# Optimization experiments

Hardware: AMD Instinct MI355X
Metric: run time of the kernel (lower is better)

Reference implementation:

```python
import jax, jax.numpy as jnp
import numpy as np

EPS = 1e-12  # torch F.normalize eps


def unfold(x, ksize, pad):
    # torch F.unfold equivalent: [B,C,H,W] -> [B, C*k*k, L], channel-major ordering
    patches = jax.lax.conv_general_dilated_patches(
        x, (ksize, ksize), (1, 1), [(pad, pad), (pad, pad)],
        dimension_numbers=('NCHW', 'OIHW', 'NCHW'))
    B, CKK, Hp, Wp = patches.shape
    return patches.reshape(B, CKK, Hp * Wp)


def fold(patches, C, ksize, H, W, pad):
    # torch F.fold equivalent (stride 1): overlap-add of [B, C*k*k, H*W] -> [B,C,H,W]
    B = patches.shape[0]
    p = patches.reshape(B, C, ksize, ksize, H, W)
    out = jnp.zeros((B, C, H + 2 * pad, W + 2 * pad), patches.dtype)
    for di in range(ksize):
        for dj in range(ksize):
            out = out.at[:, :, di:di + H, dj:dj + W].add(p[:, :, di, dj])
    return out[:, :, pad:pad + H, pad:pad + W]


def setup_inputs() -> dict:
    key = jax.random.key(0)
    ks = jax.random.split(key, 4)
    B, C, H, W = 2, 512, 64, 64
    D, CIN = 256, 512 * 9  # embed: Linear(tdim*8*3*3 -> tdim*4), tdim=64
    return {
        'query': jax.random.normal(ks[0], (B, C, H, W), dtype=jnp.float32),
        'key': jax.random.normal(ks[1], (B, C, H, W), dtype=jnp.float32),
        'value': jax.random.normal(ks[2], (B, C, H, W), dtype=jnp.float32),
        'W_embed': jax.random.normal(ks[3], (D, CIN), dtype=jnp.float32) * 0.02,
        'k': 3,
    }


def reference(query, key, value, W_embed, k):
    B, Cv, H, W = value.shape
    # patch embed: unfold -> linear (no bias)
    q_unf = unfold(query, k, k // 2)                       # [B, C*k*k, L]
    k_unf = unfold(key, k, k // 2)                         # [B, C*k*k, L]
    k_emb = jnp.einsum('bcl,dc->bld', k_unf, W_embed)      # [B, L, D]
    q_emb = jnp.einsum('bcl,dc->bdl', q_unf, W_embed)      # [B, D, L]
    # cosine correlation
    k_n = k_emb / jnp.maximum(jnp.linalg.norm(k_emb, axis=2, keepdims=True), EPS)
    q_n = q_emb / jnp.maximum(jnp.linalg.norm(q_emb, axis=1, keepdims=True), EPS)
    corr = jnp.einsum('bld,bdm->blm', k_n, q_n)            # [B, L_key, L_query]
    corr_value = jnp.max(corr, axis=1)                     # [B, L]
    corr_argmax = jnp.argmax(corr, axis=1)                 # [B, L]
    # swap(V=value, idx=corr_argmax, s=1, k=k)
    s = 1
    temph = s * k + H * s - H - s                          # = k - 1
    tempw = s * k + W * s - W - s
    ph = max(temph // 2 + temph % 2, 1)
    pw = max(tempw // 2 + tempw % 2, 1)
    v_unf = unfold(value, k, ph)                           # [B, Cv*k*k, L] (ph==pw for square)
    t_unf = jnp.take_along_axis(v_unf, corr_argmax[:, None, :], axis=2)
    divisor = fold(jnp.ones_like(t_unf), Cv, k, H, W, ph)
    T = fold(t_unf, Cv, k, H, W, ph) / divisor             # [B, Cv, H, W]
    S = corr_value.reshape(B, 1, H, W)
    return S, T
```

## Files before the change

kernel.cpp:

```cpp
#include <hip/hip_runtime.h>
#include <hip/hip_bf16.h>
#include <stdint.h>
#include <math.h>

#define BB 2
#define CC 512
#define HH 64
#define WW 64
#define LL 4096
#define DD 256
#define CIN 4608
#define NG 144

typedef _Float16 half_t;
typedef __attribute__((ext_vector_type(8))) _Float16 f16x8;
typedef __attribute__((ext_vector_type(4))) _Float16 f16x4;
typedef __attribute__((ext_vector_type(4))) float f32x4;

__global__ __launch_bounds__(256) void presplit(const float* __restrict__ query,
                                                const float* __restrict__ key,
                                                char* __restrict__ img_ts) {
    __shared__ float tile[32][65];
    int img = blockIdx.y;
    int y   = blockIdx.x;
    const float* src = ((img >> 1) ? key : query) + (size_t)(img & 1) * CC * LL + y * WW;
    char* dstbase = img_ts + ((size_t)img * 64 + y) * (16 * 64 * 128);
    int t = threadIdx.x;
    int xl = t & 63, c4 = t >> 6;
    int xw = t >> 2, fsw = t & 3;
    for (int cc = 0; cc < 16; ++cc) {
#pragma unroll
        for (int j = 0; j < 8; ++j) {
            int cl = c4 + j * 4;
            tile[cl][xl] = src[(size_t)(cc * 32 + cl) * LL + xl];
        }
        __syncthreads();
        f16x8 h8, l8;
#pragma unroll
        for (int j = 0; j < 8; ++j) {
            float v = tile[fsw * 8 + j][xw];
            half_t h = (half_t)v;
            h8[j] = h; l8[j] = (half_t)(v - (float)h);
        }
        char* p = dstbase + (size_t)cc * 8192 + xw * 128;
        int swz = (xw & 7) << 4;
        *(f16x8*)(p + ((fsw * 16) ^ swz)) = h8;
        *(f16x8*)(p + ((64 + fsw * 16) ^ swz)) = l8;
        __syncthreads();
    }
}

__global__ __launch_bounds__(256) void splitW2b(const float* __restrict__ W,
                                                char* __restrict__ Wst) {
    int i = blockIdx.x * 256 + threadIdx.x;
    if (i >= NG * DD * 4) return;
    int g  = i >> 10;
    int r  = i & 1023;
    int d  = r >> 2;
    int fs = r & 3;
    int cc = g / 9, o = g - cc * 9;
    const float* src = W + (size_t)d * CIN;
    f16x8 h8, l8;
#pragma unroll
    for (int j = 0; j < 8; j++) {
        float w = src[(cc * 32 + fs * 8 + j) * 9 + o];
        half_t h = (half_t)w;
        h8[j] = h;
        l8[j] = (half_t)(w - (float)h);
    }
    size_t base = (size_t)g * 32768 + d * 128;
    int sw = (d & 7) << 4;
    *(f16x8*)(Wst + base + ((fs * 16) ^ sw)) = h8;
    *(f16x8*)(Wst + base + ((64 + fs * 16) ^ sw)) = l8;
}

#define GATE() do { asm volatile("s_waitcnt vmcnt(0) lgkmcnt(0)" ::: "memory"); \
                    __builtin_amdgcn_s_barrier(); \
                    __builtin_amdgcn_sched_barrier(0); } while (0)

__global__ __launch_bounds__(512) void embed_mfma(const char* __restrict__ img_ts,
                                                  const char* __restrict__ Wst,
                                                  const char* __restrict__ zp,
                                                  char* __restrict__ qemb,
                                                  char* __restrict__ kemb) {
    __shared__ char sW[2][32768];
    __shared__ char sB[2][32768];
    __shared__ float red[4][64];
    __shared__ float invn[64];

    int iid = blockIdx.y;
    int b = iid & 1, type = iid >> 1;
    int y = blockIdx.x;
    int l0 = y * 64;
    int t = threadIdx.x;
    int w = t >> 6, lane = t & 63;
    int wr = w >> 1, wc = w & 1;
    int fr = lane & 15, fs = lane >> 4;

    const char* imgb = img_ts + (size_t)iid * (64 * 16 * 64 * 128);
    const char *ps0, *ps1, *ps2, *ps3;
    int pb0, pb1, pb2, pb3;
#define PREP(c, PS, PB)                                                 \
    {                                                                   \
        int q = (c) * 512 + t;                                          \
        int di = q / 528;                                               \
        int rem = q - di * 528;                                         \
        int xi = rem >> 3, sub = rem & 7;                               \
        int xg = xi - 1, yg = y + di - 1;                               \
        bool ok = (di < 3) && (yg >= 0) && (yg < 64) && (xg >= 0) && (xg < 64); \
        PS = ok ? imgb + (size_t)yg * 131072 + (size_t)xg * 128 + (sub * 16) \
                : zp + ((q & 255) * 16);                                \
        PB = ok ? 8192 : 0;                                             \
    }
    PREP(0, ps0, pb0); PREP(1, ps1, pb1); PREP(2, ps2, pb2); PREP(3, ps3, pb3);

    const char* pW = Wst;

#define DMAW(dst)                                                       \
    do {                                                                \
        _Pragma("unroll")                                               \
        for (int c = 0; c < 4; c++)                                     \
            __builtin_amdgcn_global_load_lds(                           \
                (const __attribute__((address_space(1))) void*)(pW + c * 8192 + t * 16), \
                (__attribute__((address_space(3))) void*)((dst) + c * 8192 + t * 16), 16, 0, 0); \
        pW += 32768;                                                    \
    } while (0)

#define DMAB(dst)                                                       \
    do {                                                                \
        __builtin_amdgcn_global_load_lds((const __attribute__((address_space(1))) void*)ps0, \
            (__attribute__((address_space(3))) void*)((dst) + t * 16), 16, 0, 0); \
        __builtin_amdgcn_global_load_lds((const __attribute__((address_space(1))) void*)ps1, \
            (__attribute__((address_space(3))) void*)((dst) + 8192 + t * 16), 16, 0, 0); \
        __builtin_amdgcn_global_load_lds((const __attribute__((address_space(1))) void*)ps2, \
            (__attribute__((address_space(3))) void*)((dst) + 16384 + t * 16), 16, 0, 0); \
        __builtin_amdgcn_global_load_lds((const __attribute__((address_space(1))) void*)ps3, \
            (__attribute__((address_space(3))) void*)((dst) + 24576 + t * 16), 16, 0, 0); \
        ps0 += pb0; ps1 += pb1; ps2 += pb2; ps3 += pb3;                 \
    } while (0)

#define READA(AH, AL, wbuf)                                             \
    do {                                                                \
        _Pragma("unroll")                                               \
        for (int rg = 0; rg < 4; rg++) {                                \
            int dl = wr * 64 + rg * 16 + fr;                            \
            int sw_ = (dl & 7) << 4;                                    \
            const char* rowp = (const char*)(wbuf) + dl * 128;          \
            AH[rg] = *(const f16x8*)(rowp + ((fs * 16) ^ sw_));         \
            AL[rg] = *(const f16x8*)(rowp + ((64 + fs * 16) ^ sw_));    \
        }                                                               \
    } while (0)

#define READB(BH, BL, bbuf, di_, dj_)                                   \
    do {                                                                \
        _Pragma("unroll")                                               \
        for (int cg = 0; cg < 2; cg++) {                                \
            int xi = wc * 32 + cg * 16 + fr + (dj_);                    \
            int sw_ = ((xi - 1) & 7) << 4;                              \
            const char* rowp = (const char*)(bbuf) + (di_) * 8448 + xi * 128; \
            BH[cg] = *(const f16x8*)(rowp + ((fs * 16) ^ sw_));         \
            BL[cg] = *(const f16x8*)(rowp + ((64 + fs * 16) ^ sw_));    \
        }                                                               \
    } while (0)

#define DOMFMA(AH, AL, BH, BL)                                          \
    do {                                                                \
        _Pragma("unroll")                                               \
        for (int rg = 0; rg < 4; rg++)                                  \
            _Pragma("unroll")                                           \
            for (int cg = 0; cg < 2; cg++)                              \
                acc[rg][cg] = __builtin_amdgcn_mfma_f32_16x16x32_f16(AH[rg], BH[cg], acc[rg][cg], 0, 0, 0); \
        _Pragma("unroll")                                               \
        for (int rg = 0; rg < 4; rg++)                                  \
            _Pragma("unroll")                                           \
            for (int cg = 0; cg < 2; cg++) {                            \
                acc[rg][cg] = __builtin_amdgcn_mfma_f32_16x16x32_f16(AH[rg], BL[cg], acc[rg][cg], 0, 0, 0); \
                acc[rg][cg] = __builtin_amdgcn_mfma_f32_16x16x32_f16(AL[rg], BH[cg], acc[rg][cg], 0, 0, 0); \
            }                                                           \
    } while (0)

    f32x4 acc[4][2];
#pragma unroll
    for (int rg = 0; rg < 4; rg++)
#pragma unroll
        for (int cg = 0; cg < 2; cg++) acc[rg][cg] = (f32x4){0.f, 0.f, 0.f, 0.f};

    f16x8 ah0[4], al0[4], bh0[2], bl0[2];
    f16x8 ah1[4], al1[4], bh1[2], bl1[2];

    char* wb0 = &sW[0][0]; char* wb1 = &sW[1][0];
    char* b0 = &sB[0][0];  char* b1 = &sB[1][0];

    DMAB(b0);
    DMAW(wb0);
    GATE();
    READA(ah0, al0, wb0);
    READB(bh0, bl0, b0, 0, 0);
    DMAW(wb1);
    DMAB(b1);
    __builtin_amdgcn_sched_barrier(0);

    int o = 1, issued = 2;
    char* bcur = b0;
    char* bnext = b0;

#define HALF(AHr, ALr, BHr, BLr, WRD, WWR, AHm, ALm, BHm, BLm)          \
    GATE();                                                             \
    READA(AHr, ALr, WRD);                                               \
    {                                                                   \
        int di_ = (o >= 6) ? 2 : (o >= 3) ? 1 : 0;                      \
        int dj_ = o - di_ * 3;                                          \
        READB(BHr, BLr, bcur, di_, dj_);                                \
    }                                                                   \
    DMAW(WWR);                                                          \
    if (o == 0 && issued < 16) {                                        \
        DMAB(bnext);                                                    \
        bnext = (bnext == b0) ? b1 : b0;                                \
        issued++;                                                       \
    }                                                                   \
    o++; if (o == 9) { o = 0; bcur = (bcur == b0) ? b1 : b0; }          \
    __builtin_amdgcn_sched_barrier(0);                                  \
    DOMFMA(AHm, ALm, BHm, BLm);

#pragma unroll 1
    for (int i = 0; i < 71; ++i) {
        HALF(ah1, al1, bh1, bl1, wb1, wb0, ah0, al0, bh0, bl0)
        HALF(ah0, al0, bh0, bl0, wb0, wb1, ah1, al1, bh1, bl1)
    }
    GATE();
    READA(ah1, al1, wb1);
    READB(bh1, bl1, bcur, 2, 2);
    __builtin_amdgcn_sched_barrier(0);
    DOMFMA(ah0, al0, bh0, bl0);
    DOMFMA(ah1, al1, bh1, bl1);
#undef HALF

    float ss[2] = {0.f, 0.f};
#pragma unroll
    for (int rg = 0; rg < 4; rg++)
#pragma unroll
        for (int cg = 0; cg < 2; cg++)
#pragma unroll
            for (int r = 0; r < 4; r++) ss[cg] += acc[rg][cg][r] * acc[rg][cg][r];
#pragma unroll
    for (int cg = 0; cg < 2; cg++) {
        ss[cg] += __shfl_xor(ss[cg], 16);
        ss[cg] += __shfl_xor(ss[cg], 32);
    }
    if (lane < 16) {
        red[wr][wc * 32 + lane] = ss[0];
        red[wr][wc * 32 + 16 + lane] = ss[1];
    }
    __syncthreads();
    if (t < 64) {
        float s = red[0][t] + red[1][t] + red[2][t] + red[3][t];
        invn[t] = 1.0f / fmaxf(sqrtf(s), 1e-12f);
    }
    __syncthreads();

    char* e = (type == 0) ? qemb : kemb;
#pragma unroll
    for (int cg = 0; cg < 2; cg++) {
        int lloc = wc * 32 + cg * 16 + fr;
        float sc = invn[lloc];
        int l = l0 + lloc;
        char* rowp = e + ((size_t)b * LL + l) * 1024;
        int swb = (l & 7) << 4;
#pragma unroll
        for (int rg = 0; rg < 4; rg++) {
            int d0 = wr * 64 + rg * 16 + fs * 4;
            f16x4 h4, l4;
#pragma unroll
            for (int r = 0; r < 4; r++) {
                float v = acc[rg][cg][r] * sc;
                half_t h = (half_t)v;
                h4[r] = h;
                l4[r] = (half_t)(v - (float)h);
            }
            int itb = d0 >> 5;
            int fsc = (d0 >> 3) & 3;
            int sub = (d0 & 7) * 2;
            *(f16x4*)(rowp + itb * 128 + ((fsc * 16) ^ swb) + sub) = h4;
            *(f16x4*)(rowp + itb * 128 + ((64 + fsc * 16) ^ swb) + sub) = l4;
        }
    }
#undef PREP
#undef DMAW
#undef DMAB
#undef READA
#undef READB
#undef DOMFMA
}

__global__ void init_packed(unsigned long long* p, int n) {
    int i = blockIdx.x * 256 + threadIdx.x;
    if (i < n) p[i] = 0ull;
}

__global__ __launch_bounds__(256, 2) void corr_max_mfma(const char* __restrict__ kemb,
                                                        const char* __restrict__ qemb,
                                                        unsigned long long* __restrict__ packed) {
    __shared__ char sA[2][16384];
    __shared__ char sBq[2][16384];

    int b  = blockIdx.z;
    int l0 = blockIdx.y * 128;
    int m0 = blockIdx.x * 128;
    int t  = threadIdx.x;
    int w = t >> 6, lane = t & 63;
    int wr = w >> 1, wc = w & 1;
    int fr = lane & 15, fs = lane >> 4;

    const char* Abase = kemb + ((size_t)b * LL + l0) * 1024;
    const char* Bbase = qemb + ((size_t)b * LL + m0) * 1024;

    f32x4 acc[4][4];
#pragma unroll
    for (int i = 0; i < 4; i++)
#pragma unroll
        for (int j = 0; j < 4; j++) acc[i][j] = (f32x4){0.f, 0.f, 0.f, 0.f};

#define DMA2(bufi, itv)                                                   \
    do {                                                                  \
        _Pragma("unroll")                                                 \
        for (int c = 0; c < 4; c++) {                                     \
            int idx = c * 4096 + t * 16;                                  \
            int row = idx >> 7, offb = idx & 127;                         \
            __builtin_amdgcn_global_load_lds(                             \
                (const __attribute__((address_space(1))) void*)(Abase + (size_t)row * 1024 + (itv) * 128 + offb), \
                (__attribute__((address_space(3))) void*)(&sA[bufi][idx]), 16, 0, 0); \
        }                                                                 \
        _Pragma("unroll")                                                 \
        for (int c = 0; c < 4; c++) {                                     \
            int idx = c * 4096 + t * 16;                                  \
            int row = idx >> 7, offb = idx & 127;                         \
            __builtin_amdgcn_global_load_lds(                             \
                (const __attribute__((address_space(1))) void*)(Bbase + (size_t)row * 1024 + (itv) * 128 + offb), \
                (__attribute__((address_space(3))) void*)(&sBq[bufi][idx]), 16, 0, 0); \
        }                                                                 \
    } while (0)

    DMA2(0, 0);

    f16x8 ah[4], al[4], bh[4], bl[4];
    for (int it = 0; it < 8; ++it) {
        asm volatile("s_waitcnt vmcnt(0) lgkmcnt(0)" ::: "memory");
        __builtin_amdgcn_s_barrier();
        __builtin_amdgcn_sched_barrier(0);
        if (it < 7) DMA2((it + 1) & 1, it + 1);
        __builtin_amdgcn_sched_barrier(0);
        const char* sa = sA[it & 1];
        const char* sb = sBq[it & 1];
#pragma unroll
        for (int rg = 0; rg < 4; rg++) {
            int r = wr * 64 + rg * 16 + fr;
            const char* rp = sa + r * 128;
            int sw_ = (r & 7) << 4;
            ah[rg] = *(const f16x8*)(rp + ((fs * 16) ^ sw_));
            al[rg] = *(const f16x8*)(rp + ((64 + fs * 16) ^ sw_));
        }
#pragma unroll
        for (int cg = 0; cg < 4; cg++) {
            int r = wc * 64 + cg * 16 + fr;
            const char* rp = sb + r * 128;
            int sw_ = (r & 7) << 4;
            bh[cg] = *(const f16x8*)(rp + ((fs * 16) ^ sw_));
            bl[cg] = *(const f16x8*)(rp + ((64 + fs * 16) ^ sw_));
        }
#pragma unroll
        for (int rg = 0; rg < 4; rg++)
#pragma unroll
            for (int cg = 0; cg < 4; cg++)
                acc[rg][cg] = __builtin_amdgcn_mfma_f32_16x16x32_f16(ah[rg], bh[cg], acc[rg][cg], 0, 0, 0);
#pragma unroll
        for (int rg = 0; rg < 4; rg++)
#pragma unroll
            for (int cg = 0; cg < 4; cg++) {
                acc[rg][cg] = __builtin_amdgcn_mfma_f32_16x16x32_f16(ah[rg], bl[cg], acc[rg][cg], 0, 0, 0);
                acc[rg][cg] = __builtin_amdgcn_mfma_f32_16x16x32_f16(al[rg], bh[cg], acc[rg][cg], 0, 0, 0);
            }
    }
#undef DMA2

#pragma unroll
    for (int cg = 0; cg < 4; cg++) {
        unsigned long long best = 0ull;
#pragma unroll
        for (int rg = 0; rg < 4; rg++) {
#pragma unroll
            for (int r = 0; r < 4; r++) {
                unsigned u = __float_as_uint(acc[rg][cg][r]);
                u = (u & 0x80000000u) ? ~u : (u | 0x80000000u);
                int l = l0 + wr * 64 + rg * 16 + fs * 4 + r;
                unsigned long long p = ((unsigned long long)u << 32) | (unsigned)(4095 - l);
                best = (p > best) ? p : best;
            }
        }
        unsigned long long oo;
        oo = __shfl_xor(best, 16); best = (oo > best) ? oo : best;
        oo = __shfl_xor(best, 32); best = (oo > best) ? oo : best;
        if (lane < 16)
            atomicMax(&packed[(size_t)b * LL + m0 + wc * 64 + cg * 16 + lane], best);
    }
}

__global__ void decode_packed(const unsigned long long* __restrict__ packed,
                              float* __restrict__ S_out, int* __restrict__ arg) {
    int i = blockIdx.x * 256 + threadIdx.x;
    if (i < BB * LL) {
        unsigned long long p = packed[i];
        unsigned u = (unsigned)(p >> 32);
        unsigned bits = (u & 0x80000000u) ? (u & 0x7FFFFFFFu) : ~u;
        S_out[i] = __uint_as_float(bits);
        arg[i] = 4095 - (int)(unsigned)(p & 0xFFFFFFFFull);
    }
}

__global__ __launch_bounds__(256) void transpose_mat(const float* __restrict__ src,
                                                     float* __restrict__ dst,
                                                     int R, int Cc) {
    __shared__ float tile[32][33];
    size_t boff = (size_t)blockIdx.z * R * Cc;
    int bx = blockIdx.x;
    int by = blockIdx.y;
    int tx = threadIdx.x & 31;
    int ty = threadIdx.x >> 5;
    const float* s = src + boff;
    float* d = dst + boff;
#pragma unroll
    for (int i = 0; i < 4; i++) {
        int r = by * 32 + ty + i * 8;
        int c = bx * 32 + tx;
        tile[ty + i * 8][tx] = s[(size_t)r * Cc + c];
    }
    __syncthreads();
#pragma unroll
    for (int i = 0; i < 4; i++) {
        int c = bx * 32 + ty + i * 8;
        int r = by * 32 + tx;
        d[(size_t)c * R + r] = tile[tx][ty + i * 8];
    }
}

__global__ __launch_bounds__(256) void gather_fold(const float* __restrict__ value_t,
                                                   const int* __restrict__ arg,
                                                   float* __restrict__ T_t) {
    int b = blockIdx.y;
    int pix = blockIdx.x;
    int y = pix >> 6, x = pix & 63;
    int t = threadIdx.x;
    float2 acc = make_float2(0.f, 0.f);
    int cnty = (y == 0 || y == HH - 1) ? 2 : 3;
    int cntx = (x == 0 || x == WW - 1) ? 2 : 3;
    const int* ab = arg + b * LL;
    const float* vb = value_t + (size_t)b * LL * CC;
#pragma unroll
    for (int di = 0; di < 3; di++) {
        int my = y + 1 - di;
        if (my < 0 || my >= HH) continue;
#pragma unroll
        for (int dj = 0; dj < 3; dj++) {
            int mx = x + 1 - dj;
            if (mx < 0 || mx >= WW) continue;
            int a = ab[my * WW + mx];
            int ay = a >> 6, ax = a & 63;
            int vy = ay + di - 1, vx = ax + dj - 1;
            if (vy < 0 || vy >= HH || vx < 0 || vx >= WW) continue;
            float2 v = *(const float2*)&vb[((size_t)(vy * WW + vx)) * CC + t * 2];
            acc.x += v.x; acc.y += v.y;
        }
    }
    float inv = 1.0f / (float)(cnty * cntx);
    acc.x *= inv; acc.y *= inv;
    *(float2*)&T_t[((size_t)b * LL + pix) * CC + t * 2] = acc;
}

extern "C" void kernel_launch(void* const* d_in, const int* in_sizes, int n_in,
                              void* d_out, int out_size, void* d_ws, size_t ws_size,
                              hipStream_t stream) {
    const float* query = (const float*)d_in[0];
    const float* key   = (const float*)d_in[1];
    const float* value = (const float*)d_in[2];
    const float* Wemb  = (const float*)d_in[3];

    float* out   = (float*)d_out;
    float* S_out = out;
    float* T_out = out + BB * LL;

    char* ws = (char*)d_ws;
    char* img_ts = ws;
    char* Wst    = ws + 33554432;
    char* qemb   = ws + 38273024;
    char* kemb   = ws + 46661632;
    unsigned long long* packed = (unsigned long long*)(ws + 55050240);
    char* zp     = ws + 55115776;
    int*  arg    = (int*)(ws + 55119872);
    float* val_t = (float*)ws;
    float* T_t   = (float*)(ws + 16777216);

    init_packed   <<<dim3(34), 256, 0, stream>>>(packed, 8704);
    presplit      <<<dim3(64, 4), 256, 0, stream>>>(query, key, img_ts);
    splitW2b      <<<dim3(576), 256, 0, stream>>>(Wemb, Wst);
    embed_mfma    <<<dim3(64, 4), 512, 0, stream>>>(img_ts, Wst, zp, qemb, kemb);
    corr_max_mfma <<<dim3(32, 32, 2), 256, 0, stream>>>(kemb, qemb, packed);
    decode_packed <<<dim3(32), 256, 0, stream>>>(packed, S_out, arg);
    transpose_mat <<<dim3(128, 16, 2), 256, 0, stream>>>(value, val_t, CC, LL);
    gather_fold   <<<dim3(4096, 2), 256, 0, stream>>>(val_t, arg, T_t);
    transpose_mat <<<dim3(16, 128, 2), 256, 0, stream>>>(T_t, T_out, LL, CC);
}
```

Baseline: 229.3 us.

## Split embed GEMM over K with two-row tiles and separate normalize kernel

The embed GEMM now gives each block two image rows (128 positions) and half of the channel range (split-K over blockIdx.z). Each block writes fp32 partial sums to a workspace buffer, and a new norm_split kernel adds the two halves, L2-normalizes and writes the hi/lo fp16 split layout. The main loop also drops the double-buffered register ping-pong for a simpler single-stage loop with a barrier after each step. The aim is more B-tile reuse per W load and the same block count with a larger per-block tile. The cost is an extra kernel launch, a round trip of the fp32 partials through memory, and less overlap between LDS reads and MFMA.

```diff
diff --git a/kernel.cpp b/kernel.cpp
--- a/kernel.cpp
+++ b/kernel.cpp
@@ -78,115 +78,113 @@
                     __builtin_amdgcn_s_barrier(); \
                     __builtin_amdgcn_sched_barrier(0); } while (0)
 
-__global__ __launch_bounds__(512) void embed_mfma(const char* __restrict__ img_ts,
-                                                  const char* __restrict__ Wst,
-                                                  const char* __restrict__ zp,
-                                                  char* __restrict__ qemb,
-                                                  char* __restrict__ kemb) {
+__global__ __launch_bounds__(512, 1) void embed_mfma(const char* __restrict__ img_ts,
+                                                     const char* __restrict__ Wst,
+                                                     const char* __restrict__ zp,
+                                                     float* __restrict__ part) {
     __shared__ char sW[2][32768];
-    __shared__ char sB[2][32768];
-    __shared__ float red[4][64];
-    __shared__ float invn[64];
+    __shared__ char sB[2][33792];
 
     int iid = blockIdx.y;
-    int b = iid & 1, type = iid >> 1;
-    int y = blockIdx.x;
-    int l0 = y * 64;
+    int ks  = blockIdx.z;
+    int lt  = blockIdx.x;
+    int y0  = lt * 2;
     int t = threadIdx.x;
     int w = t >> 6, lane = t & 63;
     int wr = w >> 1, wc = w & 1;
     int fr = lane & 15, fs = lane >> 4;
 
-    const char* imgb = img_ts + (size_t)iid * (64 * 16 * 64 * 128);
-    const char *ps0, *ps1, *ps2, *ps3;
-    int pb0, pb1, pb2, pb3;
-#define PREP(c, PS, PB)                                                 \
+    const char* imgb = img_ts + (size_t)iid * (64 * 16 * 64 * 128) + (size_t)ks * 65536;
+    const char *ps0, *ps1, *ps2, *ps3, *ps4;
+    int pb0, pb1, pb2, pb3, pb4;
+#define PREP(qv, PS, PB)                                                \
     {                                                                   \
-        int q = (c) * 512 + t;                                          \
-        int di = q / 528;                                               \
-        int rem = q - di * 528;                                         \
+        int q = (qv);                                                   \
+        int ri = q / 528;                                               \
+        int rem = q - ri * 528;                                         \
         int xi = rem >> 3, sub = rem & 7;                               \
-        int xg = xi - 1, yg = y + di - 1;                               \
-        bool ok = (di < 3) && (yg >= 0) && (yg < 64) && (xg >= 0) && (xg < 64); \
-        PS = ok ? imgb + (size_t)yg * 131072 + (size_t)xg * 128 + (sub * 16) \
+        int xg = xi - 1, yg = y0 - 1 + ri;                              \
+        bool ok = (yg >= 0) && (yg < 64) && (xg >= 0) && (xg < 64);     \
+        PS = ok ? imgb + (size_t)yg * 131072 + (size_t)xg * 128 + sub * 16 \
                 : zp + ((q & 255) * 16);                                \
         PB = ok ? 8192 : 0;                                             \
     }
-    PREP(0, ps0, pb0); PREP(1, ps1, pb1); PREP(2, ps2, pb2); PREP(3, ps3, pb3);
-
-    const char* pW = Wst;
+    PREP(t, ps0, pb0); PREP(512 + t, ps1, pb1); PREP(1024 + t, ps2, pb2);
+    PREP(1536 + t, ps3, pb3); PREP(2048 + t, ps4, pb4);
+
+    const char* pW = Wst + (size_t)ks * 72 * 32768;
+
+#define GLL(src, dst)                                                   \
+    __builtin_amdgcn_global_load_lds(                                   \
+        (const __attribute__((address_space(1))) void*)(src),           \
+        (__attribute__((address_space(3))) void*)(dst), 16, 0, 0)
 
 #define DMAW(dst)                                                       \
     do {                                                                \
         _Pragma("unroll")                                               \
         for (int c = 0; c < 4; c++)                                     \
-            __builtin_amdgcn_global_load_lds(                           \
-                (const __attribute__((address_space(1))) void*)(pW + c * 8192 + t * 16), \
-                (__attribute__((address_space(3))) void*)((dst) + c * 8192 + t * 16), 16, 0, 0); \
+            GLL(pW + c * 8192 + t * 16, (dst) + c * 8192 + t * 16);     \
         pW += 32768;                                                    \
     } while (0)
 
 #define DMAB(dst)                                                       \
     do {                                                                \
-        __builtin_amdgcn_global_load_lds((const __attribute__((address_space(1))) void*)ps0, \
-            (__attribute__((address_space(3))) void*)((dst) + t * 16), 16, 0, 0); \
-        __builtin_amdgcn_global_load_lds((const __attribute__((address_space(1))) void*)ps1, \
-            (__attribute__((address_space(3))) void*)((dst) + 8192 + t * 16), 16, 0, 0); \
-        __builtin_amdgcn_global_load_lds((const __attribute__((address_space(1))) void*)ps2, \
-            (__attribute__((address_space(3))) void*)((dst) + 16384 + t * 16), 16, 0, 0); \
-        __builtin_amdgcn_global_load_lds((const __attribute__((address_space(1))) void*)ps3, \
-            (__attribute__((address_space(3))) void*)((dst) + 24576 + t * 16), 16, 0, 0); \
-        ps0 += pb0; ps1 += pb1; ps2 += pb2; ps3 += pb3;                 \
+        GLL(ps0, (dst) + t * 16);                                       \
+        GLL(ps1, (dst) + 8192 + t * 16);                                \
+        GLL(ps2, (dst) + 16384 + t * 16);                               \
+        GLL(ps3, (dst) + 24576 + t * 16);                               \
+        if (t < 64) GLL(ps4, (dst) + 32768 + t * 16);                   \
+        ps0 += pb0; ps1 += pb1; ps2 += pb2; ps3 += pb3; ps4 += pb4;     \
     } while (0)
 
-#define READA(AH, AL, wbuf)                                             \
+#define READA(wbuf)                                                     \
     do {                                                                \
         _Pragma("unroll")                                               \
         for (int rg = 0; rg < 4; rg++) {                                \
             int dl = wr * 64 + rg * 16 + fr;                            \
             int sw_ = (dl & 7) << 4;                                    \
             const char* rowp = (const char*)(wbuf) + dl * 128;          \
-            AH[rg] = *(const f16x8*)(rowp + ((fs * 16) ^ sw_));         \
-            AL[rg] = *(const f16x8*)(rowp + ((64 + fs * 16) ^ sw_));    \
+            ah[rg] = *(const f16x8*)(rowp + ((fs * 16) ^ sw_));         \
+            al[rg] = *(const f16x8*)(rowp + ((64 + fs * 16) ^ sw_));    \
         }                                                               \
     } while (0)
 
-#define READB(BH, BL, bbuf, di_, dj_)                                   \
+#define READB(bbuf, di_, dj_)                                           \
     do {                                                                \
+        int ri = wc + (di_);                                            \
         _Pragma("unroll")                                               \
-        for (int cg = 0; cg < 2; cg++) {                                \
-            int xi = wc * 32 + cg * 16 + fr + (dj_);                    \
+        for (int cg = 0; cg < 4; cg++) {                                \
+            int xi = cg * 16 + fr + (dj_);                              \
             int sw_ = ((xi - 1) & 7) << 4;                              \
-            const char* rowp = (const char*)(bbuf) + (di_) * 8448 + xi * 128; \
-            BH[cg] = *(const f16x8*)(rowp + ((fs * 16) ^ sw_));         \
-            BL[cg] = *(const f16x8*)(rowp + ((64 + fs * 16) ^ sw_));    \
+            const char* rowp = (const char*)(bbuf) + ri * 8448 + xi * 128; \
+            bh[cg] = *(const f16x8*)(rowp + ((fs * 16) ^ sw_));         \
+            bl[cg] = *(const f16x8*)(rowp + ((64 + fs * 16) ^ sw_));    \
         }                                                               \
     } while (0)
 
-#define DOMFMA(AH, AL, BH, BL)                                          \
+#define DOMFMA()                                                        \
     do {                                                                \
         _Pragma("unroll")                                               \
         for (int rg = 0; rg < 4; rg++)                                  \
             _Pragma("unroll")                                           \
-            for (int cg = 0; cg < 2; cg++)                              \
-                acc[rg][cg] = __builtin_amdgcn_mfma_f32_16x16x32_f16(AH[rg], BH[cg], acc[rg][cg], 0, 0, 0); \
+            for (int cg = 0; cg < 4; cg++)                              \
+                acc[rg][cg] = __builtin_amdgcn_mfma_f32_16x16x32_f16(ah[rg], bh[cg], acc[rg][cg], 0, 0, 0); \
         _Pragma("unroll")                                               \
         for (int rg = 0; rg < 4; rg++)                                  \
             _Pragma("unroll")                                           \
-            for (int cg = 0; cg < 2; cg++) {                            \
-                acc[rg][cg] = __builtin_amdgcn_mfma_f32_16x16x32_f16(AH[rg], BL[cg], acc[rg][cg], 0, 0, 0); \
-                acc[rg][cg] = __builtin_amdgcn_mfma_f32_16x16x32_f16(AL[rg], BH[cg], acc[rg][cg], 0, 0, 0); \
+            for (int cg = 0; cg < 4; cg++) {                            \
+                acc[rg][cg] = __builtin_amdgcn_mfma_f32_16x16x32_f16(ah[rg], bl[cg], acc[rg][cg], 0, 0, 0); \
+                acc[rg][cg] = __builtin_amdgcn_mfma_f32_16x16x32_f16(al[rg], bh[cg], acc[rg][cg], 0, 0, 0); \
             }                                                           \
     } while (0)
 
-    f32x4 acc[4][2];
+    f32x4 acc[4][4];
 #pragma unroll
     for (int rg = 0; rg < 4; rg++)
 #pragma unroll
-        for (int cg = 0; cg < 2; cg++) acc[rg][cg] = (f32x4){0.f, 0.f, 0.f, 0.f};
-
-    f16x8 ah0[4], al0[4], bh0[2], bl0[2];
-    f16x8 ah1[4], al1[4], bh1[2], bl1[2];
+        for (int cg = 0; cg < 4; cg++) acc[rg][cg] = (f32x4){0.f, 0.f, 0.f, 0.f};
+
+    f16x8 ah[4], al[4], bh[4], bl[4];
 
     char* wb0 = &sW[0][0]; char* wb1 = &sW[1][0];
     char* b0 = &sB[0][0];  char* b1 = &sB[1][0];
@@ -194,102 +192,106 @@
     DMAB(b0);
     DMAW(wb0);
     GATE();
-    READA(ah0, al0, wb0);
-    READB(bh0, bl0, b0, 0, 0);
-    DMAW(wb1);
-    DMAB(b1);
-    __builtin_amdgcn_sched_barrier(0);
-
-    int o = 1, issued = 2;
-    char* bcur = b0;
-    char* bnext = b0;
-
-#define HALF(AHr, ALr, BHr, BLr, WRD, WWR, AHm, ALm, BHm, BLm)          \
-    GATE();                                                             \
-    READA(AHr, ALr, WRD);                                               \
-    {                                                                   \
-        int di_ = (o >= 6) ? 2 : (o >= 3) ? 1 : 0;                      \
-        int dj_ = o - di_ * 3;                                          \
-        READB(BHr, BLr, bcur, di_, dj_);                                \
-    }                                                                   \
-    DMAW(WWR);                                                          \
-    if (o == 0 && issued < 16) {                                        \
-        DMAB(bnext);                                                    \
-        bnext = (bnext == b0) ? b1 : b0;                                \
-        issued++;                                                       \
-    }                                                                   \
-    o++; if (o == 9) { o = 0; bcur = (bcur == b0) ? b1 : b0; }          \
-    __builtin_amdgcn_sched_barrier(0);                                  \
-    DOMFMA(AHm, ALm, BHm, BLm);
+
+    char* wcur = wb0; char* wnext = wb1;
+    char* bcur = b0;  char* bnext = b1;
+    int o = 0, ccl = 0;
 
 #pragma unroll 1
-    for (int i = 0; i < 71; ++i) {
-        HALF(ah1, al1, bh1, bl1, wb1, wb0, ah0, al0, bh0, bl0)
-        HALF(ah0, al0, bh0, bl0, wb0, wb1, ah1, al1, bh1, bl1)
-    }
-    GATE();
-    READA(ah1, al1, wb1);
-    READB(bh1, bl1, bcur, 2, 2);
-    __builtin_amdgcn_sched_barrier(0);
-    DOMFMA(ah0, al0, bh0, bl0);
-    DOMFMA(ah1, al1, bh1, bl1);
-#undef HALF
-
-    float ss[2] = {0.f, 0.f};
+    for (int g = 0; g < 72; ++g) {
+        int di_ = (o >= 6) ? 2 : (o >= 3) ? 1 : 0;
+        int dj_ = o - di_ * 3;
+        READA(wcur);
+        READB(bcur, di_, dj_);
+        if (g < 71) DMAW(wnext);
+        if (o == 8 && ccl < 7) DMAB(bnext);
+        __builtin_amdgcn_sched_barrier(0);
+        DOMFMA();
+        GATE();
+        { char* tp = wcur; wcur = wnext; wnext = tp; }
+        if (o == 8) { char* tp = bcur; bcur = bnext; bnext = tp; o = 0; ccl++; }
+        else o++;
+    }
+
+    float* pt = part + (((size_t)iid * 32 + lt) * 2 + ks) * 32768;
 #pragma unroll
     for (int rg = 0; rg < 4; rg++)
 #pragma unroll
-        for (int cg = 0; cg < 2; cg++)
-#pragma unroll
-            for (int r = 0; r < 4; r++) ss[cg] += acc[rg][cg][r] * acc[rg][cg][r];
-#pragma unroll
-    for (int cg = 0; cg < 2; cg++) {
-        ss[cg] += __shfl_xor(ss[cg], 16);
-        ss[cg] += __shfl_xor(ss[cg], 32);
-    }
-    if (lane < 16) {
-        red[wr][wc * 32 + lane] = ss[0];
-        red[wr][wc * 32 + 16 + lane] = ss[1];
-    }
-    __syncthreads();
-    if (t < 64) {
-        float s = red[0][t] + red[1][t] + red[2][t] + red[3][t];
-        invn[t] = 1.0f / fmaxf(sqrtf(s), 1e-12f);
-    }
-    __syncthreads();
-
-    char* e = (type == 0) ? qemb : kemb;
-#pragma unroll
-    for (int cg = 0; cg < 2; cg++) {
-        int lloc = wc * 32 + cg * 16 + fr;
-        float sc = invn[lloc];
-        int l = l0 + lloc;
-        char* rowp = e + ((size_t)b * LL + l) * 1024;
-        int swb = (l & 7) << 4;
-#pragma unroll
-        for (int rg = 0; rg < 4; rg++) {
+        for (int cg = 0; cg < 4; cg++) {
+            int l = wc * 64 + cg * 16 + fr;
             int d0 = wr * 64 + rg * 16 + fs * 4;
-            f16x4 h4, l4;
-#pragma unroll
-            for (int r = 0; r < 4; r++) {
-                float v = acc[rg][cg][r] * sc;
-                half_t h = (half_t)v;
-                h4[r] = h;
-                l4[r] = (half_t)(v - (float)h);
-            }
-            int itb = d0 >> 5;
-            int fsc = (d0 >> 3) & 3;
-            int sub = (d0 & 7) * 2;
-            *(f16x4*)(rowp + itb * 128 + ((fsc * 16) ^ swb) + sub) = h4;
-            *(f16x4*)(rowp + itb * 128 + ((64 + fsc * 16) ^ swb) + sub) = l4;
-        }
-    }
+#pragma unroll
+            for (int r = 0; r < 4; r++)
+                pt[(d0 + r) * 128 + l] = acc[rg][cg][r];
+        }
 #undef PREP
+#undef GLL
 #undef DMAW
 #undef DMAB
 #undef READA
 #undef READB
 #undef DOMFMA
+}
+
+__global__ __launch_bounds__(256) void norm_split(const float* __restrict__ part,
+                                                  char* __restrict__ qemb,
+                                                  char* __restrict__ kemb) {
+    __shared__ float sm[4][64];
+    __shared__ float invn[64];
+    __shared__ char stage[64][1040];
+
+    int iid = blockIdx.y;
+    int bx  = blockIdx.x;
+    int lt  = bx >> 1, lh2 = bx & 1;
+    const float* p0 = part + (((size_t)iid * 32 + lt) * 2 + 0) * 32768 + lh2 * 64;
+    const float* p1 = p0 + 32768;
+    int t = threadIdx.x;
+    int ll = t & 63, dq = t >> 6;
+
+    float sq = 0.f;
+    for (int dd = 0; dd < 64; ++dd) {
+        int d = dq * 64 + dd;
+        float v = p0[d * 128 + ll] + p1[d * 128 + ll];
+        sq += v * v;
+    }
+    sm[dq][ll] = sq;
+    __syncthreads();
+    if (t < 64) {
+        float s = sm[0][t] + sm[1][t] + sm[2][t] + sm[3][t];
+        invn[t] = 1.0f / fmaxf(sqrtf(s), 1e-12f);
+    }
+    __syncthreads();
+
+    float sc = invn[ll];
+    int swb = (ll & 7) << 4;
+    for (int oc = 0; oc < 8; ++oc) {
+        int d0 = dq * 64 + oc * 8;
+        f16x8 h8, l8;
+#pragma unroll
+        for (int j = 0; j < 8; ++j) {
+            int d = d0 + j;
+            float v = (p0[d * 128 + ll] + p1[d * 128 + ll]) * sc;
+            half_t h = (half_t)v;
+            h8[j] = h;
+            l8[j] = (half_t)(v - (float)h);
+        }
+        int itb = d0 >> 5;
+        int fsc = (d0 >> 3) & 3;
+        *(f16x8*)&stage[ll][itb * 128 + ((fsc * 16) ^ swb)] = h8;
+        *(f16x8*)&stage[ll][itb * 128 + ((64 + fsc * 16) ^ swb)] = l8;
+    }
+    __syncthreads();
+
+    int b = iid & 1, type = iid >> 1;
+    char* e = (type ? kemb : qemb);
+    int rr = t >> 2, c0 = t & 3;
+    char* erow = e + ((size_t)b * LL + lt * 128 + lh2 * 64 + rr) * 1024;
+    const char* srow = &stage[rr][0];
+#pragma unroll
+    for (int c = 0; c < 16; ++c) {
+        int cj = c0 + c * 4;
+        *(float4*)(erow + cj * 16) = *(const float4*)(srow + cj * 16);
+    }
 }
 
 __global__ void init_packed(unsigned long long* p, int n) {
@@ -488,20 +490,22 @@
     float* T_out = out + BB * LL;
 
     char* ws = (char*)d_ws;
-    char* img_ts = ws;
-    char* Wst    = ws + 33554432;
-    char* qemb   = ws + 38273024;
-    char* kemb   = ws + 46661632;
-    unsigned long long* packed = (unsigned long long*)(ws + 55050240);
-    char* zp     = ws + 55115776;
-    int*  arg    = (int*)(ws + 55119872);
-    float* val_t = (float*)ws;
-    float* T_t   = (float*)(ws + 16777216);
+    char*  img_ts = ws;
+    char*  Wst    = ws + 33554432;
+    float* part   = (float*)(ws + 38273024);
+    char*  qemb   = ws + 71827456;
+    char*  kemb   = ws + 80216064;
+    unsigned long long* packed = (unsigned long long*)(ws + 88604672);
+    char*  zp     = ws + 88670208;
+    int*   arg    = (int*)(ws + 88674304);
+    float* val_t  = (float*)(ws + 38273024);
+    float* T_t    = (float*)(ws + 38273024 + 16777216);
 
     init_packed   <<<dim3(34), 256, 0, stream>>>(packed, 8704);
     presplit      <<<dim3(64, 4), 256, 0, stream>>>(query, key, img_ts);
     splitW2b      <<<dim3(576), 256, 0, stream>>>(Wemb, Wst);
-    embed_mfma    <<<dim3(64, 4), 512, 0, stream>>>(img_ts, Wst, zp, qemb, kemb);
+    embed_mfma    <<<dim3(32, 4, 2), 512, 0, stream>>>(img_ts, Wst, zp, part);
+    norm_split    <<<dim3(64, 4), 256, 0, stream>>>(part, qemb, kemb);
     corr_max_mfma <<<dim3(32, 32, 2), 256, 0, stream>>>(kemb, qemb, packed);
     decode_packed <<<dim3(32), 256, 0, stream>>>(packed, S_out, arg);
     transpose_mat <<<dim3(128, 16, 2), 256, 0, stream>>>(value, val_t, CC, LL);
```

Measured after the change: 221.7 us. 1.03x faster.
